# Optimization experiments

Measured on AMD Instinct MI355X. Metric: run time of the kernel, lower is better.

The kernel has to match this reference:

```python
import jax, jax.numpy as jnp
import numpy as np

N, E = 50000, 800000
D_IN, D_H, D_OUT = 256, 256, 128
EPS = 1e-5

def _p(key, shape, scale=0.05):
    return jax.random.normal(key, shape, dtype=jnp.float32) * scale

def setup_inputs():
    key = jax.random.key(0)
    ks = jax.random.split(key, 20)
    inp = {
        'x': jax.random.normal(ks[0], (N, D_IN), dtype=jnp.float32),
        'edge_index': jax.random.randint(ks[1], (2, E), 0, N, dtype=jnp.int64),
        'edge_weight': jax.random.uniform(ks[2], (E,), dtype=jnp.float32),
        # node_transform: Linear(D_IN,D_H) -> ReLU -> Dropout -> Linear(D_H,D_H) -> LayerNorm
        'W_nt1': _p(ks[3], (D_IN, D_H)), 'b_nt1': jnp.zeros((D_H,), jnp.float32),
        'W_nt2': _p(ks[4], (D_H, D_H)), 'b_nt2': jnp.zeros((D_H,), jnp.float32),
        'ln_g': jnp.ones((D_H,), jnp.float32), 'ln_b': jnp.zeros((D_H,), jnp.float32),
        # 3 hidden GCNConv layers (stacked) + BatchNorm affine params
        'Wc': _p(ks[5], (3, D_H, D_H)), 'bc': jnp.zeros((3, D_H), jnp.float32),
        'bn_g': jnp.ones((3, D_H), jnp.float32), 'bn_b': jnp.zeros((3, D_H), jnp.float32),
        # final GCNConv hidden -> output
        'Wc_last': _p(ks[6], (D_H, D_OUT)), 'bc_last': jnp.zeros((D_OUT,), jnp.float32),
    }
    return inp

def _gcn_conv(x, W, b, row, col, norm, n):
    # PyG GCNConv: linear transform, then edge-weighted normalized scatter-add, then bias
    xw = x @ W                                   # [n, d_out]
    msg = norm[:, None] * xw[row]                # gather along sources [E+n, d_out]
    agg = jax.ops.segment_sum(msg, col, num_segments=n)
    return agg + b

def _gcn_forward(x, edge_index, edge_weight, W_nt1, b_nt1, W_nt2, b_nt2, ln_g, ln_b,
                 Wc, bc, bn_g, bn_b, Wc_last, bc_last):
    n = x.shape[0]
    row, col = edge_index[0], edge_index[1]
    loops = jnp.arange(n, dtype=row.dtype)
    row_f = jnp.concatenate([row, loops])
    col_f = jnp.concatenate([col, loops])
    w_f = jnp.concatenate([edge_weight, jnp.ones((n,), x.dtype)])  # self-loop weight 1
    # symmetric normalization: D^{-1/2} (A+I) D^{-1/2}
    deg = jax.ops.segment_sum(w_f, col_f, num_segments=n)
    dis = jnp.where(deg > 0, jax.lax.rsqrt(deg), 0.0)
    norm = dis[row_f] * w_f * dis[col_f]

    # node_transform (dropout inactive in eval)
    h = jax.nn.relu(x @ W_nt1 + b_nt1)
    h = h @ W_nt2 + b_nt2
    mu = h.mean(-1, keepdims=True)
    var = h.var(-1, keepdims=True)
    node_features = (h - mu) * jax.lax.rsqrt(var + EPS) * ln_g + ln_b

    cur = x
    for i in range(3):  # fixed small layer loop
        xc = _gcn_conv(cur, Wc[i], bc[i], row_f, col_f, norm, n)
        m = xc.mean(0)
        v = xc.var(0)  # biased variance, matching torch BN training math
        xc = (xc - m) * jax.lax.rsqrt(v + EPS) * bn_g[i] + bn_b[i]
        xc = jax.nn.relu(xc)
        cur = xc + cur if cur.shape[1] == xc.shape[1] else xc
        if i == 0:
            cur = cur + node_features
        # F.dropout with training=False is identity
    node_emb = _gcn_conv(cur, Wc_last, bc_last, row_f, col_f, norm, n)
    graph_emb = node_emb.mean(0, keepdims=True)  # global_mean_pool, single graph
    return node_emb, graph_emb

def reference(x, edge_index, edge_weight, W_nt1, b_nt1, W_nt2, b_nt2, ln_g, ln_b,
              Wc, bc, bn_g, bn_b, Wc_last, bc_last):
    return _gcn_forward(x, edge_index, edge_weight, W_nt1, b_nt1, W_nt2, b_nt2,
                        ln_g, ln_b, Wc, bc, bn_g, bn_b, Wc_last, bc_last)
```

## Files before the change

### kernel.cpp

```cpp
#include <hip/hip_runtime.h>

#define EPSV 1e-5f

typedef __attribute__((ext_vector_type(8))) short v8s;
typedef __attribute__((ext_vector_type(4))) float v4f;

__device__ __forceinline__ unsigned short f2bf(float f){
  unsigned int u = __float_as_uint(f);
  u += 0x7FFF + ((u >> 16) & 1);
  return (unsigned short)(u >> 16);
}
__device__ __forceinline__ void bf2x(unsigned int u, float& lo, float& hi){
  lo = __uint_as_float(u << 16);
  hi = __uint_as_float(u & 0xffff0000u);
}

__global__ void k_init(float* deg, int* cnt, int N){
  int i = blockIdx.x*256 + threadIdx.x;
  if (i < N){ deg[i] = 1.0f; cnt[i] = 0; }
}

__global__ void k_deg(const int* ei, const float* ew, float* deg, int* cnt, int E){
  int e = blockIdx.x*256 + threadIdx.x;
  if (e < E){
    int c = ei[E + e];
    atomicAdd(&deg[c], ew[e]);
    atomicAdd(&cnt[c], 1);
  }
}

__global__ void k_dis(const float* deg, float* dis, int N){
  int i = blockIdx.x*256 + threadIdx.x;
  if (i < N) dis[i] = rsqrtf(deg[i]);
}

__global__ __launch_bounds__(256) void k_scan1(const int* cnt, int* part, int N){
  const int t = threadIdx.x, b = blockIdx.x;
  const int base = b*1024 + t*4;
  int4 v = make_int4(0,0,0,0);
  if (base + 3 < N) v = *(const int4*)(cnt + base);
  else {
    if (base   < N) v.x = cnt[base];
    if (base+1 < N) v.y = cnt[base+1];
    if (base+2 < N) v.z = cnt[base+2];
    if (base+3 < N) v.w = cnt[base+3];
  }
  int s = v.x + v.y + v.z + v.w;
  __shared__ int sm[256];
  sm[t] = s;
  __syncthreads();
  for (int off = 128; off > 0; off >>= 1){
    if (t < off) sm[t] += sm[t + off];
    __syncthreads();
  }
  if (t == 0) part[b] = sm[0];
}

__global__ __launch_bounds__(64) void k_scan2(int* part, int* offs, int NB, int N){
  const int t = threadIdx.x;
  int orig = (t < NB) ? part[t] : 0;
  int v = orig;
  for (int off = 1; off < 64; off <<= 1){
    int u = __shfl_up(v, off, 64);
    if (t >= off) v += u;
  }
  if (t < NB) part[t] = v - orig;
  if (t == 63) offs[N] = v;
}

__global__ __launch_bounds__(256) void k_scan3(int* cnt, const int* part, int* offs, int N){
  const int t = threadIdx.x, b = blockIdx.x;
  const int base = b*1024 + t*4;
  int4 v = make_int4(0,0,0,0);
  if (base + 3 < N) v = *(const int4*)(cnt + base);
  else {
    if (base   < N) v.x = cnt[base];
    if (base+1 < N) v.y = cnt[base+1];
    if (base+2 < N) v.z = cnt[base+2];
    if (base+3 < N) v.w = cnt[base+3];
  }
  int s = v.x + v.y + v.z + v.w;
  __shared__ int sm[256];
  sm[t] = s;
  __syncthreads();
  for (int off = 1; off < 256; off <<= 1){
    int u = (t >= off) ? sm[t - off] : 0;
    __syncthreads();
    sm[t] += u;
    __syncthreads();
  }
  int run = part[b] + sm[t] - s;
  if (base   < N) offs[base]   = run; run += v.x;
  if (base+1 < N) offs[base+1] = run; run += v.y;
  if (base+2 < N) offs[base+2] = run; run += v.z;
  if (base+3 < N) offs[base+3] = run;
  if (base + 3 < N) *(int4*)(cnt + base) = make_int4(0,0,0,0);
  else {
    if (base   < N) cnt[base]   = 0;
    if (base+1 < N) cnt[base+1] = 0;
    if (base+2 < N) cnt[base+2] = 0;
  }
}

__global__ void k_bucket(const int* ei, const float* ew, const float* dis, const int* offs,
                         int* cursor, int2* ep, int E){
  int e = blockIdx.x*256 + threadIdx.x;
  if (e < E){
    int r = ei[e], c = ei[E + e];
    float nrm = dis[r] * ew[e] * dis[c];
    int pos = offs[c] + atomicAdd(&cursor[c], 1);
    ep[pos] = make_int2(r, __float_as_int(nrm));
  }
}

__global__ void k_wt(const float* W1, const float* W2, const float* Wc, const float* Wl,
                     unsigned short* WT){
  int t = blockIdx.x*256 + threadIdx.x;
  int k = t >> 8, n = t & 255;
  WT[0*65536 + n*256 + k] = f2bf(W1[k*256 + n]);
  WT[1*65536 + n*256 + k] = f2bf(W2[k*256 + n]);
  WT[2*65536 + n*256 + k] = f2bf(Wc[0*65536 + k*256 + n]);
  WT[3*65536 + n*256 + k] = f2bf(Wc[1*65536 + k*256 + n]);
  WT[4*65536 + n*256 + k] = f2bf(Wc[2*65536 + k*256 + n]);
  if (n < 128) WT[5*65536 + n*256 + k] = f2bf(Wl[k*128 + n]);
}

template<bool ABF16, bool OUTBF16, bool BIAS, bool RELU>
__global__ __launch_bounds__(256, 3) void k_gemm(const void* Ap, const unsigned short* WT,
    const float* bias, void* Cp, int M, int Nout){
  __shared__ unsigned short As[128][40];
  __shared__ unsigned short Bs[128][40];
  const int tid  = threadIdx.x;
  const int lane = tid & 63, wv = tid >> 6;
  const int wm = wv >> 1, wn = wv & 1;
  const int quad = lane >> 4, m16 = lane & 15;
  const int bm = blockIdx.x, bn = blockIdx.y;
  const int srow = tid >> 1, sseg = (tid & 1) * 16;
  const int arow_g = min(bm*128 + srow, M - 1);

  v4f acc[4][4];
  #pragma unroll
  for (int a = 0; a < 4; a++)
    #pragma unroll
    for (int b = 0; b < 4; b++) acc[a][b] = (v4f)(0.0f);

  const float* Af = (const float*)Ap;
  const unsigned short* Ab = (const unsigned short*)Ap;

  for (int ks = 0; ks < 256; ks += 32){
    __syncthreads();
    if constexpr (ABF16){
      const unsigned short* src = Ab + (size_t)arow_g*256 + ks + sseg;
      uint4 u0 = *(const uint4*)(src);
      uint4 u1 = *(const uint4*)(src + 8);
      *(uint4*)&As[srow][sseg]     = u0;
      *(uint4*)&As[srow][sseg + 8] = u1;
    } else {
      const float* src = Af + (size_t)arow_g*256 + ks + sseg;
      float4 v0 = *(const float4*)(src + 0);
      float4 v1 = *(const float4*)(src + 4);
      float4 v2 = *(const float4*)(src + 8);
      float4 v3 = *(const float4*)(src + 12);
      uint4 q0, q1;
      q0.x = f2bf(v0.x) | ((unsigned)f2bf(v0.y) << 16);
      q0.y = f2bf(v0.z) | ((unsigned)f2bf(v0.w) << 16);
      q0.z = f2bf(v1.x) | ((unsigned)f2bf(v1.y) << 16);
      q0.w = f2bf(v1.z) | ((unsigned)f2bf(v1.w) << 16);
      q1.x = f2bf(v2.x) | ((unsigned)f2bf(v2.y) << 16);
      q1.y = f2bf(v2.z) | ((unsigned)f2bf(v2.w) << 16);
      q1.z = f2bf(v3.x) | ((unsigned)f2bf(v3.y) << 16);
      q1.w = f2bf(v3.z) | ((unsigned)f2bf(v3.w) << 16);
      *(uint4*)&As[srow][sseg]     = q0;
      *(uint4*)&As[srow][sseg + 8] = q1;
    }
    {
      const unsigned short* src = WT + (size_t)(bn*128 + srow)*256 + ks + sseg;
      uint4 u0 = *(const uint4*)(src);
      uint4 u1 = *(const uint4*)(src + 8);
      *(uint4*)&Bs[srow][sseg]     = u0;
      *(uint4*)&Bs[srow][sseg + 8] = u1;
    }
    __syncthreads();

    v8s af[4], bfr[4];
    #pragma unroll
    for (int tm = 0; tm < 4; tm++) af[tm]  = *(const v8s*)&As[wm*64 + tm*16 + m16][quad*8];
    #pragma unroll
    for (int tn = 0; tn < 4; tn++) bfr[tn] = *(const v8s*)&Bs[wn*64 + tn*16 + m16][quad*8];
    #pragma unroll
    for (int tm = 0; tm < 4; tm++)
      #pragma unroll
      for (int tn = 0; tn < 4; tn++)
        acc[tm][tn] = __builtin_amdgcn_mfma_f32_16x16x32_bf16(af[tm], bfr[tn], acc[tm][tn], 0, 0, 0);
  }

  #pragma unroll
  for (int tn = 0; tn < 4; tn++){
    int col = bn*128 + wn*64 + tn*16 + m16;
    float bv = BIAS ? bias[col] : 0.0f;
    #pragma unroll
    for (int tm = 0; tm < 4; tm++){
      int row0 = bm*128 + wm*64 + tm*16 + quad*4;
      #pragma unroll
      for (int r = 0; r < 4; r++){
        int row = row0 + r;
        if (row < M){
          float v = acc[tm][tn][r] + bv;
          if (RELU) v = fmaxf(v, 0.0f);
          if (OUTBF16) ((unsigned short*)Cp)[(size_t)row*Nout + col] = f2bf(v);
          else         ((float*)Cp)[(size_t)row*Nout + col] = v;
        }
      }
    }
  }
}

__global__ __launch_bounds__(256) void k_ln(const float* h, const float* g, const float* b,
                                            unsigned short* nf, int N){
  const int lane = threadIdx.x & 63, wv = threadIdx.x >> 6;
  const int i = blockIdx.x*4 + wv;
  if (i >= N) return;
  const float* row = h + (size_t)i*256;
  float4 v = *(const float4*)(row + lane*4);
  float s = v.x + v.y + v.z + v.w;
  float q = v.x*v.x + v.y*v.y + v.z*v.z + v.w*v.w;
  for (int off = 32; off > 0; off >>= 1){
    s += __shfl_xor(s, off, 64);
    q += __shfl_xor(q, off, 64);
  }
  float mean = s * (1.0f/256.0f);
  float var  = q * (1.0f/256.0f) - mean*mean;
  float rs = rsqrtf(var + EPSV);
  int c = lane*4;
  ushort4 st;
  st.x = f2bf((v.x - mean)*rs*g[c+0] + b[c+0]);
  st.y = f2bf((v.y - mean)*rs*g[c+1] + b[c+1]);
  st.z = f2bf((v.z - mean)*rs*g[c+2] + b[c+2]);
  st.w = f2bf((v.w - mean)*rs*g[c+3] + b[c+3]);
  *(ushort4*)(nf + (size_t)i*256 + c) = st;
}

template<int D, bool BIAS>
__global__ __launch_bounds__(256) void k_agg(const unsigned short* xw, const int2* ep,
    const int* offs, const float* dis, const float* bias, float* out, int N){
  constexpr int V = D / 64;
  const int lane = threadIdx.x & 63, wv = threadIdx.x >> 6;
  const int i = blockIdx.x*4 + wv;
  if (i >= N) return;
  float acc[V];
  float dsi = dis[i];
  float coef = dsi * dsi;
  {
    const unsigned short* r = xw + (size_t)i*D + lane*V;
    if constexpr (V == 4){
      uint2 u = *(const uint2*)r;
      float a,b2,c,d; bf2x(u.x,a,b2); bf2x(u.y,c,d);
      acc[0]=coef*a; acc[1]=coef*b2; acc[2]=coef*c; acc[3]=coef*d;
    } else {
      unsigned int u = *(const unsigned int*)r;
      float a,b2; bf2x(u,a,b2);
      acc[0]=coef*a; acc[1]=coef*b2;
    }
  }
  const int e0 = offs[i], e1 = offs[i+1];
  for (int eb = e0; eb < e1; eb += 64){
    const int nb = min(64, e1 - eb);
    int2 pl = make_int2(0, 0);
    if (eb + lane < e1) pl = ep[eb + lane];
    int j = 0;
    for (; j + 8 <= nb; j += 8){
      int s0,s1,s2,s3,s4,s5,s6,s7;
      float n0,n1,n2,n3,n4,n5,n6,n7;
      s0=__shfl(pl.x,j+0,64); s1=__shfl(pl.x,j+1,64); s2=__shfl(pl.x,j+2,64); s3=__shfl(pl.x,j+3,64);
      s4=__shfl(pl.x,j+4,64); s5=__shfl(pl.x,j+5,64); s6=__shfl(pl.x,j+6,64); s7=__shfl(pl.x,j+7,64);
      n0=__int_as_float(__shfl(pl.y,j+0,64)); n1=__int_as_float(__shfl(pl.y,j+1,64));
      n2=__int_as_float(__shfl(pl.y,j+2,64)); n3=__int_as_float(__shfl(pl.y,j+3,64));
      n4=__int_as_float(__shfl(pl.y,j+4,64)); n5=__int_as_float(__shfl(pl.y,j+5,64));
      n6=__int_as_float(__shfl(pl.y,j+6,64)); n7=__int_as_float(__shfl(pl.y,j+7,64));
      if constexpr (V == 4){
        uint2 u0 = *(const uint2*)(xw + (size_t)s0*D + lane*V);
        uint2 u1 = *(const uint2*)(xw + (size_t)s1*D + lane*V);
        uint2 u2 = *(const uint2*)(xw + (size_t)s2*D + lane*V);
        uint2 u3 = *(const uint2*)(xw + (size_t)s3*D + lane*V);
        uint2 u4 = *(const uint2*)(xw + (size_t)s4*D + lane*V);
        uint2 u5 = *(const uint2*)(xw + (size_t)s5*D + lane*V);
        uint2 u6 = *(const uint2*)(xw + (size_t)s6*D + lane*V);
        uint2 u7 = *(const uint2*)(xw + (size_t)s7*D + lane*V);
        float a,b2,c,d;
        bf2x(u0.x,a,b2); bf2x(u0.y,c,d);
        acc[0]=fmaf(n0,a,acc[0]); acc[1]=fmaf(n0,b2,acc[1]); acc[2]=fmaf(n0,c,acc[2]); acc[3]=fmaf(n0,d,acc[3]);
        bf2x(u1.x,a,b2); bf2x(u1.y,c,d);
        acc[0]=fmaf(n1,a,acc[0]); acc[1]=fmaf(n1,b2,acc[1]); acc[2]=fmaf(n1,c,acc[2]); acc[3]=fmaf(n1,d,acc[3]);
        bf2x(u2.x,a,b2); bf2x(u2.y,c,d);
        acc[0]=fmaf(n2,a,acc[0]); acc[1]=fmaf(n2,b2,acc[1]); acc[2]=fmaf(n2,c,acc[2]); acc[3]=fmaf(n2,d,acc[3]);
        bf2x(u3.x,a,b2); bf2x(u3.y,c,d);
        acc[0]=fmaf(n3,a,acc[0]); acc[1]=fmaf(n3,b2,acc[1]); acc[2]=fmaf(n3,c,acc[2]); acc[3]=fmaf(n3,d,acc[3]);
        bf2x(u4.x,a,b2); bf2x(u4.y,c,d);
        acc[0]=fmaf(n4,a,acc[0]); acc[1]=fmaf(n4,b2,acc[1]); acc[2]=fmaf(n4,c,acc[2]); acc[3]=fmaf(n4,d,acc[3]);
        bf2x(u5.x,a,b2); bf2x(u5.y,c,d);
        acc[0]=fmaf(n5,a,acc[0]); acc[1]=fmaf(n5,b2,acc[1]); acc[2]=fmaf(n5,c,acc[2]); acc[3]=fmaf(n5,d,acc[3]);
        bf2x(u6.x,a,b2); bf2x(u6.y,c,d);
        acc[0]=fmaf(n6,a,acc[0]); acc[1]=fmaf(n6,b2,acc[1]); acc[2]=fmaf(n6,c,acc[2]); acc[3]=fmaf(n6,d,acc[3]);
        bf2x(u7.x,a,b2); bf2x(u7.y,c,d);
        acc[0]=fmaf(n7,a,acc[0]); acc[1]=fmaf(n7,b2,acc[1]); acc[2]=fmaf(n7,c,acc[2]); acc[3]=fmaf(n7,d,acc[3]);
      } else {
        unsigned int u0 = *(const unsigned int*)(xw + (size_t)s0*D + lane*V);
        unsigned int u1 = *(const unsigned int*)(xw + (size_t)s1*D + lane*V);
        unsigned int u2 = *(const unsigned int*)(xw + (size_t)s2*D + lane*V);
        unsigned int u3 = *(const unsigned int*)(xw + (size_t)s3*D + lane*V);
        unsigned int u4 = *(const unsigned int*)(xw + (size_t)s4*D + lane*V);
        unsigned int u5 = *(const unsigned int*)(xw + (size_t)s5*D + lane*V);
        unsigned int u6 = *(const unsigned int*)(xw + (size_t)s6*D + lane*V);
        unsigned int u7 = *(const unsigned int*)(xw + (size_t)s7*D + lane*V);
        float a,b2;
        bf2x(u0,a,b2); acc[0]=fmaf(n0,a,acc[0]); acc[1]=fmaf(n0,b2,acc[1]);
        bf2x(u1,a,b2); acc[0]=fmaf(n1,a,acc[0]); acc[1]=fmaf(n1,b2,acc[1]);
        bf2x(u2,a,b2); acc[0]=fmaf(n2,a,acc[0]); acc[1]=fmaf(n2,b2,acc[1]);
        bf2x(u3,a,b2); acc[0]=fmaf(n3,a,acc[0]); acc[1]=fmaf(n3,b2,acc[1]);
        bf2x(u4,a,b2); acc[0]=fmaf(n4,a,acc[0]); acc[1]=fmaf(n4,b2,acc[1]);
        bf2x(u5,a,b2); acc[0]=fmaf(n5,a,acc[0]); acc[1]=fmaf(n5,b2,acc[1]);
        bf2x(u6,a,b2); acc[0]=fmaf(n6,a,acc[0]); acc[1]=fmaf(n6,b2,acc[1]);
        bf2x(u7,a,b2); acc[0]=fmaf(n7,a,acc[0]); acc[1]=fmaf(n7,b2,acc[1]);
      }
    }
    for (; j < nb; j++){
      int   s0 = __shfl(pl.x, j, 64);
      float n0 = __int_as_float(__shfl(pl.y, j, 64));
      if constexpr (V == 4){
        uint2 u = *(const uint2*)(xw + (size_t)s0*D + lane*V);
        float a,b2,c,d; bf2x(u.x,a,b2); bf2x(u.y,c,d);
        acc[0]=fmaf(n0,a,acc[0]); acc[1]=fmaf(n0,b2,acc[1]);
        acc[2]=fmaf(n0,c,acc[2]); acc[3]=fmaf(n0,d,acc[3]);
      } else {
        unsigned int u = *(const unsigned int*)(xw + (size_t)s0*D + lane*V);
        float a,b2; bf2x(u,a,b2);
        acc[0]=fmaf(n0,a,acc[0]); acc[1]=fmaf(n0,b2,acc[1]);
      }
    }
  }
  float* o = out + (size_t)i*D + lane*V;
  if constexpr (V == 4){
    float4 st = make_float4(acc[0] + (BIAS?bias[lane*4+0]:0.f),
                            acc[1] + (BIAS?bias[lane*4+1]:0.f),
                            acc[2] + (BIAS?bias[lane*4+2]:0.f),
                            acc[3] + (BIAS?bias[lane*4+3]:0.f));
    *(float4*)o = st;
  } else {
    float2 st = make_float2(acc[0] + (BIAS?bias[lane*2+0]:0.f),
                            acc[1] + (BIAS?bias[lane*2+1]:0.f));
    *(float2*)o = st;
  }
}

__global__ __launch_bounds__(256) void k_stats(const float* xc, float* acc, int N){
  const int t  = threadIdx.x;
  const int c4 = t & 63;
  const int rs = t >> 6;
  const int rows = (N + gridDim.x - 1) / gridDim.x;
  const int r0 = blockIdx.x * rows;
  const int r1 = min(r0 + rows, N);
  float4 s = make_float4(0,0,0,0), q = make_float4(0,0,0,0);
  for (int r = r0 + rs; r < r1; r += 4){
    float4 v = ((const float4*)(xc + (size_t)r*256))[c4];
    s.x += v.x; s.y += v.y; s.z += v.z; s.w += v.w;
    q.x = fmaf(v.x, v.x, q.x); q.y = fmaf(v.y, v.y, q.y);
    q.z = fmaf(v.z, v.z, q.z); q.w = fmaf(v.w, v.w, q.w);
  }
  __shared__ float4 sm[512];
  sm[t] = s; sm[256 + t] = q;
  __syncthreads();
  for (int off = 128; off >= 64; off >>= 1){
    if (t < off){
      float4 a = sm[t + off];       sm[t].x += a.x; sm[t].y += a.y; sm[t].z += a.z; sm[t].w += a.w;
      float4 b = sm[256 + t + off]; sm[256+t].x += b.x; sm[256+t].y += b.y; sm[256+t].z += b.z; sm[256+t].w += b.w;
    }
    __syncthreads();
  }
  if (t < 64){
    float4 sv = sm[t], qv = sm[256 + t];
    atomicAdd(&acc[t*4+0], sv.x); atomicAdd(&acc[t*4+1], sv.y);
    atomicAdd(&acc[t*4+2], sv.z); atomicAdd(&acc[t*4+3], sv.w);
    atomicAdd(&acc[256+t*4+0], qv.x); atomicAdd(&acc[256+t*4+1], qv.y);
    atomicAdd(&acc[256+t*4+2], qv.z); atomicAdd(&acc[256+t*4+3], qv.w);
  }
}

__global__ void k_bnfin(const float* acc, const float* g, const float* b, float* ss, int N){
  int ch = threadIdx.x;
  float mean = acc[ch] / (float)N;
  float var  = acc[256 + ch] / (float)N - mean*mean;
  float sc = g[ch] * rsqrtf(var + EPSV);
  ss[ch]       = sc;
  ss[256 + ch] = b[ch] - mean * sc;
}

__global__ void k_apply(const float* xc, const float* ss, const float* resid,
                        const unsigned short* nf, float* outc, int total4){
  for (int idx = blockIdx.x*blockDim.x + threadIdx.x; idx < total4; idx += gridDim.x*blockDim.x){
    int cq = idx & 63;
    float4 v  = ((const float4*)xc)[idx];
    float4 sc = ((const float4*)ss)[cq];
    float4 sh = ((const float4*)ss)[64 + cq];
    float4 r  = ((const float4*)resid)[idx];
    float o0 = fmaxf(fmaf(v.x, sc.x, sh.x), 0.0f) + r.x;
    float o1 = fmaxf(fmaf(v.y, sc.y, sh.y), 0.0f) + r.y;
    float o2 = fmaxf(fmaf(v.z, sc.z, sh.z), 0.0f) + r.z;
    float o3 = fmaxf(fmaf(v.w, sc.w, sh.w), 0.0f) + r.w;
    if (nf){
      uint2 u = ((const uint2*)nf)[idx];
      float a,b2,c,d; bf2x(u.x,a,b2); bf2x(u.y,c,d);
      o0 += a; o1 += b2; o2 += c; o3 += d;
    }
    ((float4*)outc)[idx] = make_float4(o0, o1, o2, o3);
  }
}

__global__ __launch_bounds__(256) void k_graph(const float* ne, float* g, int N){
  const int t  = threadIdx.x;
  const int c4 = t & 31;
  const int rs = t >> 5;
  const int rows = (N + gridDim.x - 1) / gridDim.x;
  const int r0 = blockIdx.x * rows;
  const int r1 = min(r0 + rows, N);
  float4 a = make_float4(0,0,0,0);
  for (int r = r0 + rs; r < r1; r += 8){
    float4 v = ((const float4*)(ne + (size_t)r*128))[c4];
    a.x += v.x; a.y += v.y; a.z += v.z; a.w += v.w;
  }
  __shared__ float4 sm[256];
  sm[t] = a;
  __syncthreads();
  for (int off = 128; off >= 32; off >>= 1){
    if (t < off){
      float4 b = sm[t + off];
      sm[t].x += b.x; sm[t].y += b.y; sm[t].z += b.z; sm[t].w += b.w;
    }
    __syncthreads();
  }
  if (t < 32){
    float4 v = sm[t];
    float inv = 1.0f / (float)N;
    atomicAdd(&g[t*4+0], v.x*inv); atomicAdd(&g[t*4+1], v.y*inv);
    atomicAdd(&g[t*4+2], v.z*inv); atomicAdd(&g[t*4+3], v.w*inv);
  }
}

extern "C" void kernel_launch(void* const* d_in, const int* in_sizes, int n_in,
                              void* d_out, int out_size, void* d_ws, size_t ws_size,
                              hipStream_t stream){
  const float* x     = (const float*)d_in[0];
  const int*   ei    = (const int*)d_in[1];
  const float* ew    = (const float*)d_in[2];
  const float* W_nt1 = (const float*)d_in[3];
  const float* b_nt1 = (const float*)d_in[4];
  const float* W_nt2 = (const float*)d_in[5];
  const float* b_nt2 = (const float*)d_in[6];
  const float* ln_g  = (const float*)d_in[7];
  const float* ln_b  = (const float*)d_in[8];
  const float* Wc    = (const float*)d_in[9];
  const float* bn_g  = (const float*)d_in[11];
  const float* bn_b  = (const float*)d_in[12];
  const float* Wl    = (const float*)d_in[13];
  const float* bl    = (const float*)d_in[14];

  const int N = in_sizes[0] / 256;
  const int E = in_sizes[2];

  char* w = (char*)d_ws;
  size_t o = 0;
  auto alloc = [&](size_t bytes) -> void* {
    void* p = w + o;
    o = (o + bytes + 255) & ~(size_t)255;
    return p;
  };
  float* deg   = (float*)alloc((size_t)N*4);
  float* dis   = (float*)alloc((size_t)N*4);
  int*   cnt   = (int*)  alloc((size_t)N*4);
  int*   offs  = (int*)  alloc((size_t)(N+1)*4);
  int*   part  = (int*)  alloc(64*4);
  int2*  ep    = (int2*) alloc((size_t)E*8);
  unsigned short* WT = (unsigned short*)alloc((size_t)6*65536*2);
  unsigned short* xw = (unsigned short*)alloc((size_t)N*256*2);
  unsigned short* nf = (unsigned short*)alloc((size_t)N*256*2);
  float* xc   = (float*)alloc((size_t)N*256*4);
  float* cur  = (float*)alloc((size_t)N*256*4);
  float* bnacc = (float*)alloc(512*4);
  float* ss   = (float*)alloc(512*4);

  float* node_emb  = (float*)d_out;
  float* graph_emb = node_emb + (size_t)N*128;

  const int gN = (N + 255)/256, gE = (E + 255)/256, gW = (N + 3)/4;
  const int NB = (N + 1023)/1024;

  hipMemsetAsync(graph_emb, 0, 128*sizeof(float), stream);
  k_init<<<gN, 256, 0, stream>>>(deg, cnt, N);
  k_deg <<<gE, 256, 0, stream>>>(ei, ew, deg, cnt, E);
  k_dis <<<gN, 256, 0, stream>>>(deg, dis, N);
  k_scan1<<<NB, 256, 0, stream>>>(cnt, part, N);
  k_scan2<<<1, 64, 0, stream>>>(part, offs, NB, N);
  k_scan3<<<NB, 256, 0, stream>>>(cnt, part, offs, N);
  k_bucket<<<gE, 256, 0, stream>>>(ei, ew, dis, offs, cnt, ep, E);
  k_wt  <<<256, 256, 0, stream>>>(W_nt1, W_nt2, Wc, Wl, WT);

  dim3 gg((N + 127)/128, 2);
  k_gemm<false, true,  true, true ><<<gg, 256, 0, stream>>>(x,  WT + 0*65536, b_nt1, xw, N, 256);
  k_gemm<true,  false, true, false><<<gg, 256, 0, stream>>>(xw, WT + 1*65536, b_nt2, xc, N, 256);
  k_ln<<<gW, 256, 0, stream>>>(xc, ln_g, ln_b, nf, N);

  for (int i = 0; i < 3; i++){
    const float* cin = (i == 0) ? x : cur;
    k_gemm<false, true, false, false><<<gg, 256, 0, stream>>>(cin, WT + (size_t)(2+i)*65536, nullptr, xw, N, 256);
    k_agg<256, false><<<gW, 256, 0, stream>>>(xw, ep, offs, dis, nullptr, xc, N);
    hipMemsetAsync(bnacc, 0, 512*sizeof(float), stream);
    k_stats<<<512, 256, 0, stream>>>(xc, bnacc, N);
    k_bnfin<<<1, 256, 0, stream>>>(bnacc, bn_g + i*256, bn_b + i*256, ss, N);
    k_apply<<<2048, 256, 0, stream>>>(xc, ss, cin, (i == 0) ? nf : nullptr, cur, N*64);
  }

  dim3 gl((N + 127)/128, 1);
  k_gemm<false, true, false, false><<<gl, 256, 0, stream>>>(cur, WT + (size_t)5*65536, nullptr, xw, N, 128);
  k_agg<128, true><<<gW, 256, 0, stream>>>(xw, ep, offs, dis, bl, node_emb, N);
  k_graph<<<256, 256, 0, stream>>>(node_emb, graph_emb, N);
}
```

Baseline: 916.0 us.

## Pre-cast GEMM inputs to bf16 and pack degree/count into one 64-bit atomic

```diff
diff --git a/kernel.cpp b/kernel.cpp
--- a/kernel.cpp
+++ b/kernel.cpp
@@ -15,23 +15,28 @@
   hi = __uint_as_float(u & 0xffff0000u);
 }
 
-__global__ void k_init(float* deg, int* cnt, int N){
+__global__ void k_init(unsigned long long* packed, int N){
   int i = blockIdx.x*256 + threadIdx.x;
-  if (i < N){ deg[i] = 1.0f; cnt[i] = 0; }
-}
-
-__global__ void k_deg(const int* ei, const float* ew, float* deg, int* cnt, int E){
+  if (i < N) packed[i] = (1ULL << 24);
+}
+
+__global__ void k_deg(const int* ei, const float* ew, unsigned long long* packed, int E){
   int e = blockIdx.x*256 + threadIdx.x;
   if (e < E){
     int c = ei[E + e];
-    atomicAdd(&deg[c], ew[e]);
-    atomicAdd(&cnt[c], 1);
-  }
-}
-
-__global__ void k_dis(const float* deg, float* dis, int N){
+    unsigned long long inc = (1ULL << 40) | (unsigned long long)(ew[e] * 16777216.0f + 0.5f);
+    atomicAdd(&packed[c], inc);
+  }
+}
+
+__global__ void k_post(const unsigned long long* packed, float* dis, int* cnt, int N){
   int i = blockIdx.x*256 + threadIdx.x;
-  if (i < N) dis[i] = rsqrtf(deg[i]);
+  if (i < N){
+    unsigned long long p = packed[i];
+    float deg = (float)(p & ((1ULL << 40) - 1)) * (1.0f/16777216.0f);
+    dis[i] = rsqrtf(deg);
+    cnt[i] = (int)(p >> 40);
+  }
 }
 
 __global__ __launch_bounds__(256) void k_scan1(const int* cnt, int* part, int N){
@@ -113,6 +118,16 @@
   }
 }
 
+__global__ void k_cast(const float* x, unsigned short* xb, int total4){
+  int idx = blockIdx.x*256 + threadIdx.x;
+  if (idx < total4){
+    float4 v = ((const float4*)x)[idx];
+    ushort4 s;
+    s.x = f2bf(v.x); s.y = f2bf(v.y); s.z = f2bf(v.z); s.w = f2bf(v.w);
+    ((ushort4*)xb)[idx] = s;
+  }
+}
+
 __global__ void k_wt(const float* W1, const float* W2, const float* Wc, const float* Wl,
                      unsigned short* WT){
   int t = blockIdx.x*256 + threadIdx.x;
@@ -125,8 +140,8 @@
   if (n < 128) WT[5*65536 + n*256 + k] = f2bf(Wl[k*128 + n]);
 }
 
-template<bool ABF16, bool OUTBF16, bool BIAS, bool RELU>
-__global__ __launch_bounds__(256, 3) void k_gemm(const void* Ap, const unsigned short* WT,
+template<bool OUTBF16, bool BIAS, bool RELU>
+__global__ __launch_bounds__(256, 3) void k_gemm(const unsigned short* A, const unsigned short* WT,
     const float* bias, void* Cp, int M, int Nout){
   __shared__ unsigned short As[128][40];
   __shared__ unsigned short Bs[128][40];
@@ -144,34 +159,14 @@
     #pragma unroll
     for (int b = 0; b < 4; b++) acc[a][b] = (v4f)(0.0f);
 
-  const float* Af = (const float*)Ap;
-  const unsigned short* Ab = (const unsigned short*)Ap;
-
   for (int ks = 0; ks < 256; ks += 32){
     __syncthreads();
-    if constexpr (ABF16){
-      const unsigned short* src = Ab + (size_t)arow_g*256 + ks + sseg;
+    {
+      const unsigned short* src = A + (size_t)arow_g*256 + ks + sseg;
       uint4 u0 = *(const uint4*)(src);
       uint4 u1 = *(const uint4*)(src + 8);
       *(uint4*)&As[srow][sseg]     = u0;
       *(uint4*)&As[srow][sseg + 8] = u1;
-    } else {
-      const float* src = Af + (size_t)arow_g*256 + ks + sseg;
-      float4 v0 = *(const float4*)(src + 0);
-      float4 v1 = *(const float4*)(src + 4);
-      float4 v2 = *(const float4*)(src + 8);
-      float4 v3 = *(const float4*)(src + 12);
-      uint4 q0, q1;
-      q0.x = f2bf(v0.x) | ((unsigned)f2bf(v0.y) << 16);
-      q0.y = f2bf(v0.z) | ((unsigned)f2bf(v0.w) << 16);
-      q0.z = f2bf(v1.x) | ((unsigned)f2bf(v1.y) << 16);
-      q0.w = f2bf(v1.z) | ((unsigned)f2bf(v1.w) << 16);
-      q1.x = f2bf(v2.x) | ((unsigned)f2bf(v2.y) << 16);
-      q1.y = f2bf(v2.z) | ((unsigned)f2bf(v2.w) << 16);
-      q1.z = f2bf(v3.x) | ((unsigned)f2bf(v3.y) << 16);
-      q1.w = f2bf(v3.z) | ((unsigned)f2bf(v3.w) << 16);
-      *(uint4*)&As[srow][sseg]     = q0;
-      *(uint4*)&As[srow][sseg + 8] = q1;
     }
     {
       const unsigned short* src = WT + (size_t)(bn*128 + srow)*256 + ks + sseg;
@@ -395,7 +390,7 @@
 }
 
 __global__ void k_apply(const float* xc, const float* ss, const float* resid,
-                        const unsigned short* nf, float* outc, int total4){
+                        const unsigned short* nf, float* outc, unsigned short* outb, int total4){
   for (int idx = blockIdx.x*blockDim.x + threadIdx.x; idx < total4; idx += gridDim.x*blockDim.x){
     int cq = idx & 63;
     float4 v  = ((const float4*)xc)[idx];
@@ -412,6 +407,8 @@
       o0 += a; o1 += b2; o2 += c; o3 += d;
     }
     ((float4*)outc)[idx] = make_float4(o0, o1, o2, o3);
+    ushort4 s4; s4.x = f2bf(o0); s4.y = f2bf(o1); s4.z = f2bf(o2); s4.w = f2bf(o3);
+    ((ushort4*)outb)[idx] = s4;
   }
 }
 
@@ -473,15 +470,17 @@
     o = (o + bytes + 255) & ~(size_t)255;
     return p;
   };
-  float* deg   = (float*)alloc((size_t)N*4);
+  unsigned long long* packed = (unsigned long long*)alloc((size_t)N*8);
   float* dis   = (float*)alloc((size_t)N*4);
   int*   cnt   = (int*)  alloc((size_t)N*4);
   int*   offs  = (int*)  alloc((size_t)(N+1)*4);
   int*   part  = (int*)  alloc(64*4);
   int2*  ep    = (int2*) alloc((size_t)E*8);
   unsigned short* WT = (unsigned short*)alloc((size_t)6*65536*2);
-  unsigned short* xw = (unsigned short*)alloc((size_t)N*256*2);
-  unsigned short* nf = (unsigned short*)alloc((size_t)N*256*2);
+  unsigned short* xbf = (unsigned short*)alloc((size_t)N*256*2);
+  unsigned short* xw  = (unsigned short*)alloc((size_t)N*256*2);
+  unsigned short* nf  = (unsigned short*)alloc((size_t)N*256*2);
+  unsigned short* curbf = (unsigned short*)alloc((size_t)N*256*2);
   float* xc   = (float*)alloc((size_t)N*256*4);
   float* cur  = (float*)alloc((size_t)N*256*4);
   float* bnacc = (float*)alloc(512*4);
@@ -494,32 +493,34 @@
   const int NB = (N + 1023)/1024;
 
   hipMemsetAsync(graph_emb, 0, 128*sizeof(float), stream);
-  k_init<<<gN, 256, 0, stream>>>(deg, cnt, N);
-  k_deg <<<gE, 256, 0, stream>>>(ei, ew, deg, cnt, E);
-  k_dis <<<gN, 256, 0, stream>>>(deg, dis, N);
+  k_init<<<gN, 256, 0, stream>>>(packed, N);
+  k_deg <<<gE, 256, 0, stream>>>(ei, ew, packed, E);
+  k_post<<<gN, 256, 0, stream>>>(packed, dis, cnt, N);
   k_scan1<<<NB, 256, 0, stream>>>(cnt, part, N);
   k_scan2<<<1, 64, 0, stream>>>(part, offs, NB, N);
   k_scan3<<<NB, 256, 0, stream>>>(cnt, part, offs, N);
   k_bucket<<<gE, 256, 0, stream>>>(ei, ew, dis, offs, cnt, ep, E);
   k_wt  <<<256, 256, 0, stream>>>(W_nt1, W_nt2, Wc, Wl, WT);
+  k_cast<<<(N*64 + 255)/256, 256, 0, stream>>>(x, xbf, N*64);
 
   dim3 gg((N + 127)/128, 2);
-  k_gemm<false, true,  true, true ><<<gg, 256, 0, stream>>>(x,  WT + 0*65536, b_nt1, xw, N, 256);
-  k_gemm<true,  false, true, false><<<gg, 256, 0, stream>>>(xw, WT + 1*65536, b_nt2, xc, N, 256);
+  k_gemm<true,  true, true ><<<gg, 256, 0, stream>>>(xbf, WT + 0*65536, b_nt1, xw, N, 256);
+  k_gemm<false, true, false><<<gg, 256, 0, stream>>>(xw,  WT + 1*65536, b_nt2, xc, N, 256);
   k_ln<<<gW, 256, 0, stream>>>(xc, ln_g, ln_b, nf, N);
 
   for (int i = 0; i < 3; i++){
-    const float* cin = (i == 0) ? x : cur;
-    k_gemm<false, true, false, false><<<gg, 256, 0, stream>>>(cin, WT + (size_t)(2+i)*65536, nullptr, xw, N, 256);
+    const unsigned short* ain = (i == 0) ? xbf : curbf;
+    const float* rin = (i == 0) ? x : cur;
+    k_gemm<true, false, false><<<gg, 256, 0, stream>>>(ain, WT + (size_t)(2+i)*65536, nullptr, xw, N, 256);
     k_agg<256, false><<<gW, 256, 0, stream>>>(xw, ep, offs, dis, nullptr, xc, N);
     hipMemsetAsync(bnacc, 0, 512*sizeof(float), stream);
     k_stats<<<512, 256, 0, stream>>>(xc, bnacc, N);
     k_bnfin<<<1, 256, 0, stream>>>(bnacc, bn_g + i*256, bn_b + i*256, ss, N);
-    k_apply<<<2048, 256, 0, stream>>>(xc, ss, cin, (i == 0) ? nf : nullptr, cur, N*64);
+    k_apply<<<2048, 256, 0, stream>>>(xc, ss, rin, (i == 0) ? nf : nullptr, cur, curbf, N*64);
   }
 
   dim3 gl((N + 127)/128, 1);
-  k_gemm<false, true, false, false><<<gl, 256, 0, stream>>>(cur, WT + (size_t)5*65536, nullptr, xw, N, 128);
+  k_gemm<true, false, false><<<gl, 256, 0, stream>>>(curbf, WT + (size_t)5*65536, nullptr, xw, N, 128);
   k_agg<128, true><<<gW, 256, 0, stream>>>(xw, ep, offs, dis, bl, node_emb, N);
   k_graph<<<256, 256, 0, stream>>>(node_emb, graph_emb, N);
 }
```

New measurement: 877.3 us. -4.2%, faster.
